# Optimization experiments

Measured on AMD Instinct MI355X. Metric: run time of the kernel, lower is better.

Reference implementation:

```python
import jax, jax.numpy as jnp
import numpy as np

B, H, W, CIN, F, KH, KW, E = 16, 112, 112, 128, 256, 3, 3, 3


@jax.custom_vjp
def ste_sign(x):
    # larq-style ste_sign: sign with sign(0) -> +1
    return jnp.where(x >= 0, 1.0, -1.0).astype(x.dtype)

def _ste_fwd(x):
    return ste_sign(x), x

def _ste_bwd(x, g):
    # straight-through estimator, clipped to |x| <= 1
    return (g * (jnp.abs(x) <= 1).astype(g.dtype),)

ste_sign.defvjp(_ste_fwd, _ste_bwd)


def conv2d(x, k):
    return jax.lax.conv_general_dilated(
        x, k, window_strides=(1, 1), padding='VALID',
        dimension_numbers=('NHWC', 'HWIO', 'NHWC'))


def setup_inputs() -> dict:
    key = jax.random.key(0)
    k1, k2 = jax.random.split(key)
    x = jax.random.normal(k1, (B, H, W, CIN), dtype=jnp.float32)
    kernels = jax.random.normal(k2, (E, KH, KW, CIN, F), dtype=jnp.float32) * 0.1
    # alpha initialized as mean |kernel| per output filter (as in build())
    alphas = jnp.mean(jnp.abs(kernels), axis=(1, 2, 3))  # [E, F]
    return {"x": x, "kernels": kernels, "alphas": alphas}


def reference(x, kernels, alphas):
    kh, kw, cin = kernels.shape[1], kernels.shape[2], kernels.shape[3]
    D = kh * kw * cin  # db_dimension
    xq = ste_sign(x)  # binarized input (shared across estimators)
    ones_k = jnp.ones((kh, kw, cin, 1), dtype=x.dtype)
    # beta: box-filter of |x| over window and channels, divided by D -> [B,H',W']
    beta = conv2d(jnp.abs(x), ones_k)[..., 0] / D
    out = jnp.zeros((1,), dtype=x.dtype)  # broadcast accumulator
    for e in range(kernels.shape[0]):
        Z = conv2d(xq, ste_sign(kernels[e]))  # [B,H',W',F], binary conv
        K = beta[..., None] * alphas[e]       # outer(beta, alpha)
        out = out + Z * K
    return out
```

## Files before the change

### kernel.cpp

```cpp
#include <hip/hip_runtime.h>
#include <hip/hip_bf16.h>
#include <stdint.h>

#define B_   16
#define H_   112
#define W_   112
#define CIN  128
#define F_   256
#define OH   110
#define OW   110
#define MTOT (B_*OH*OW)
#define KTOT 1152
#define PIX_IN (B_*H_*W_)
#define D_INV (1.0f/1152.0f)

typedef float floatx4 __attribute__((ext_vector_type(4)));
typedef int   intx4   __attribute__((ext_vector_type(4)));

typedef __attribute__((address_space(1))) uint32_t guint;
typedef __attribute__((address_space(3))) uint32_t luint;

__device__ __forceinline__ void gld_lds16(const void* g, void* l) {
    __builtin_amdgcn_global_load_lds((guint*)g, (luint*)l, 16, 0, 0);
}

#define WST_OFF   0
#define SF_OFF    294912
#define S_OFF     295936
#define BETA_OFF  1098752
#define XQ_OFF    1873152
#define NEED_FULL (XQ_OFF + (size_t)PIX_IN*CIN)

__global__ void prep_wq(const float* __restrict__ kern, const float* __restrict__ alph,
                        int8_t* __restrict__ wst, float* __restrict__ sf) {
    int idx = blockIdx.x * 256 + threadIdx.x;
    int r = idx >> 8, f = idx & 255;
    float a0 = alph[f], a1 = alph[256 + f], a2 = alph[512 + f];
    float w = 0.f;
    float kv0 = kern[idx], kv1 = kern[294912 + idx], kv2 = kern[589824 + idx];
    w += (__float_as_uint(kv0) & 0x80000000u) ? -a0 : a0;
    w += (__float_as_uint(kv1) & 0x80000000u) ? -a1 : a1;
    w += (__float_as_uint(kv2) & 0x80000000u) ? -a2 : a2;
    float s = (a0 + a1 + a2) * (1.0f / 127.0f);
    int q = (int)__builtin_rintf(w / s);
    wst[((((r >> 6) * 2 + (f >> 7)) * 4 + ((r >> 4) & 3)) * 128 + (f & 127)) * 16 + (r & 15)]
        = (int8_t)q;
    if (r == 0) sf[f] = s;
}

__device__ __forceinline__ uint32_t pack4sign(float4 v) {
    uint32_t b0 = ((__float_as_uint(v.x) >> 31) * 0xFEu) ^ 0x01u;
    uint32_t b1 = ((__float_as_uint(v.y) >> 31) * 0xFEu) ^ 0x01u;
    uint32_t b2 = ((__float_as_uint(v.z) >> 31) * 0xFEu) ^ 0x01u;
    uint32_t b3 = ((__float_as_uint(v.w) >> 31) * 0xFEu) ^ 0x01u;
    return b0 | (b1 << 8) | (b2 << 16) | (b3 << 24);
}

__global__ void prep_x(const float* __restrict__ x, uint32_t* __restrict__ xq,
                       float* __restrict__ S, int write_xq) {
    int idx = blockIdx.x * 256 + threadIdx.x;
    float4 v = ((const float4*)x)[idx];
    if (write_xq) xq[idx] = pack4sign(v);
    float s = fabsf(v.x) + fabsf(v.y) + fabsf(v.z) + fabsf(v.w);
#pragma unroll
    for (int o = 1; o < 32; o <<= 1) s += __shfl_xor(s, o, 64);
    if ((threadIdx.x & 31) == 0) S[idx >> 5] = s;
}

__global__ void prep_beta(const float* __restrict__ S, float* __restrict__ beta) {
    int m = blockIdx.x * 256 + threadIdx.x;
    if (m >= MTOT) return;
    int b = m / (OH * OW); int r = m - b * (OH * OW);
    int oi = r / OW, oj = r - oi * OW;
    const float* sp = S + (b * H_ + oi) * W_ + oj;
    float acc = 0.f;
#pragma unroll
    for (int dh = 0; dh < 3; ++dh)
#pragma unroll
        for (int dw = 0; dw < 3; ++dw) acc += sp[dh * W_ + dw];
    beta[m] = acc * D_INV;
}

template <bool PREBIN>
__global__ __launch_bounds__(256)
void conv_main(const void* __restrict__ xin, const int8_t* __restrict__ wst,
               const float* __restrict__ sf, const float* __restrict__ beta,
               float* __restrict__ out) {
    __shared__ char smem[16384];

    const int t = threadIdx.x;
    const int l = t & 63, wv = t >> 6;
    const int quad = l >> 4, lane16 = l & 15;
    const int wm = wv >> 1, wn = wv & 1;
    const int f0 = blockIdx.x * 128;
    const int m0 = blockIdx.y * 128;

    const char* a_base[2];
    const char* b_base[2];
#pragma unroll
    for (int q = 0; q < 2; ++q) {
        int idx = q * 256 + t;
        int chunk = idx >> 7, rn = idx & 127;
        int m = m0 + rn; if (m >= MTOT) m = MTOT - 1;
        int b = m / (OH * OW); int rr = m - b * (OH * OW);
        int oi = rr / OW, oj = rr - oi * OW;
        long pix = ((long)(b * H_ + oi) * W_ + oj) * CIN;
        a_base[q] = (const char*)xin + (PREBIN ? (pix + chunk * 16)
                                               : (pix + chunk * 16) * 4);
        b_base[q] = (const char*)wst + blockIdx.x * 8192 + idx * 16;
    }

    intx4 acc[4][4];
#pragma unroll
    for (int a = 0; a < 4; ++a)
#pragma unroll
        for (int bb = 0; bb < 4; ++bb) acc[a][bb] = (intx4){0, 0, 0, 0};

    for (int ks = 0; ks < 18; ++ks) {
        int kh = ks / 6, rem = ks - kh * 6;
        int kw = rem >> 1, c0 = (rem & 1) << 6;
        int aoff = (kh * W_ + kw) * CIN + c0;
#pragma unroll
        for (int q = 0; q < 2; ++q) {
            int idx = q * 256 + t;
            if (PREBIN) {
                gld_lds16(a_base[q] + aoff, smem + idx * 16);
            } else {
                const float4* src = (const float4*)(a_base[q] + (long)aoff * 4);
                float4 v0 = src[0], v1 = src[1], v2 = src[2], v3 = src[3];
                uint4 pv = make_uint4(pack4sign(v0), pack4sign(v1),
                                      pack4sign(v2), pack4sign(v3));
                *(uint4*)(smem + idx * 16) = pv;
            }
            gld_lds16(b_base[q] + (long)ks * 16384, smem + 8192 + idx * 16);
        }
        __syncthreads();

        intx4 af[4], bf[4];
#pragma unroll
        for (int tm = 0; tm < 4; ++tm) {
            int row = wm * 64 + tm * 16 + lane16;
            af[tm] = *(const intx4*)(smem + quad * 2048 + row * 16);
        }
#pragma unroll
        for (int tn = 0; tn < 4; ++tn) {
            int col = wn * 64 + tn * 16 + lane16;
            bf[tn] = *(const intx4*)(smem + 8192 + quad * 2048 + col * 16);
        }
#pragma unroll
        for (int tm = 0; tm < 4; ++tm)
#pragma unroll
            for (int tn = 0; tn < 4; ++tn)
                acc[tm][tn] = __builtin_amdgcn_mfma_i32_16x16x64_i8(
                    af[tm], bf[tn], acc[tm][tn], 0, 0, 0);
        __syncthreads();
    }

    float sv[4];
#pragma unroll
    for (int tn = 0; tn < 4; ++tn) sv[tn] = sf[f0 + wn * 64 + tn * 16 + lane16];

#pragma unroll
    for (int tm = 0; tm < 4; ++tm) {
#pragma unroll
        for (int i = 0; i < 4; ++i) {
            int m = m0 + wm * 64 + tm * 16 + quad * 4 + i;
            if (m < MTOT) {
                float bv = beta[m];
                float* op = out + (long)m * F_ + f0 + wn * 64 + lane16;
#pragma unroll
                for (int tn = 0; tn < 4; ++tn)
                    op[tn * 16] = (float)acc[tm][tn][i] * (bv * sv[tn]);
            }
        }
    }
}

extern "C" void kernel_launch(void* const* d_in, const int* in_sizes, int n_in,
                              void* d_out, int out_size, void* d_ws, size_t ws_size,
                              hipStream_t stream) {
    const float* x    = (const float*)d_in[0];
    const float* kern = (const float*)d_in[1];
    const float* alph = (const float*)d_in[2];
    float* out = (float*)d_out;
    char* ws = (char*)d_ws;

    int8_t* wst  = (int8_t*)(ws + WST_OFF);
    float*  sf   = (float*)(ws + SF_OFF);
    float*  S    = (float*)(ws + S_OFF);
    float*  beta = (float*)(ws + BETA_OFF);
    char*   xq   = ws + XQ_OFF;
    bool prebin = ws_size >= NEED_FULL;

    hipLaunchKernelGGL(prep_wq, dim3(KTOT * F_ / 256), dim3(256), 0, stream,
                       kern, alph, wst, sf);
    hipLaunchKernelGGL(prep_x, dim3(PIX_IN * CIN / 4 / 256), dim3(256), 0, stream,
                       x, (uint32_t*)xq, S, (int)prebin);
    hipLaunchKernelGGL(prep_beta, dim3((MTOT + 255) / 256), dim3(256), 0, stream, S, beta);

    dim3 grid(2, (MTOT + 127) / 128);
    if (prebin)
        hipLaunchKernelGGL(conv_main<true>, grid, dim3(256), 0, stream,
                           (const void*)xq, wst, sf, beta, out);
    else
        hipLaunchKernelGGL(conv_main<false>, grid, dim3(256), 0, stream,
                           (const void*)x, wst, sf, beta, out);
}
```

Measured before the change: 352.4 us.

## Double-buffer LDS tiles in binary conv GEMM and remap workgroups per XCD

```diff
diff --git a/kernel.cpp b/kernel.cpp
--- a/kernel.cpp
+++ b/kernel.cpp
@@ -86,28 +86,35 @@
 void conv_main(const void* __restrict__ xin, const int8_t* __restrict__ wst,
                const float* __restrict__ sf, const float* __restrict__ beta,
                float* __restrict__ out) {
-    __shared__ char smem[16384];
+    __shared__ char smem[32768];
 
     const int t = threadIdx.x;
     const int l = t & 63, wv = t >> 6;
     const int quad = l >> 4, lane16 = l & 15;
     const int wm = wv >> 1, wn = wv & 1;
-    const int f0 = blockIdx.x * 128;
-    const int m0 = blockIdx.y * 128;
+
+    const int nwg  = gridDim.x * gridDim.y;
+    const int wgid = blockIdx.y * gridDim.x + blockIdx.x;
+    const int qn = nwg >> 3, rn = nwg & 7;
+    const int xcd = wgid & 7, ii = wgid >> 3;
+    const int nid = (xcd < rn ? xcd * (qn + 1) : rn * (qn + 1) + (xcd - rn) * qn) + ii;
+    const int f0 = (nid & 1) * 128;
+    const int m0 = (nid >> 1) * 128;
+    const int fblk = nid & 1;
 
     const char* a_base[2];
     const char* b_base[2];
 #pragma unroll
     for (int q = 0; q < 2; ++q) {
         int idx = q * 256 + t;
-        int chunk = idx >> 7, rn = idx & 127;
-        int m = m0 + rn; if (m >= MTOT) m = MTOT - 1;
+        int chunk = idx >> 7, rnn = idx & 127;
+        int m = m0 + rnn; if (m >= MTOT) m = MTOT - 1;
         int b = m / (OH * OW); int rr = m - b * (OH * OW);
         int oi = rr / OW, oj = rr - oi * OW;
         long pix = ((long)(b * H_ + oi) * W_ + oj) * CIN;
         a_base[q] = (const char*)xin + (PREBIN ? (pix + chunk * 16)
                                                : (pix + chunk * 16) * 4);
-        b_base[q] = (const char*)wst + blockIdx.x * 8192 + idx * 16;
+        b_base[q] = (const char*)wst + fblk * 8192 + idx * 16;
     }
 
     intx4 acc[4][4];
@@ -116,44 +123,65 @@
 #pragma unroll
         for (int bb = 0; bb < 4; ++bb) acc[a][bb] = (intx4){0, 0, 0, 0};
 
-    for (int ks = 0; ks < 18; ++ks) {
+    auto STAGE = [&](int ks, int buf) {
         int kh = ks / 6, rem = ks - kh * 6;
         int kw = rem >> 1, c0 = (rem & 1) << 6;
         int aoff = (kh * W_ + kw) * CIN + c0;
+        char* dst = smem + buf * 16384;
 #pragma unroll
         for (int q = 0; q < 2; ++q) {
             int idx = q * 256 + t;
             if (PREBIN) {
-                gld_lds16(a_base[q] + aoff, smem + idx * 16);
+                gld_lds16(a_base[q] + aoff, dst + idx * 16);
             } else {
                 const float4* src = (const float4*)(a_base[q] + (long)aoff * 4);
                 float4 v0 = src[0], v1 = src[1], v2 = src[2], v3 = src[3];
                 uint4 pv = make_uint4(pack4sign(v0), pack4sign(v1),
                                       pack4sign(v2), pack4sign(v3));
-                *(uint4*)(smem + idx * 16) = pv;
+                *(uint4*)(dst + idx * 16) = pv;
             }
-            gld_lds16(b_base[q] + (long)ks * 16384, smem + 8192 + idx * 16);
-        }
-        __syncthreads();
-
+            gld_lds16(b_base[q] + (long)ks * 16384, dst + 8192 + idx * 16);
+        }
+    };
+
+    STAGE(0, 0);
+
+    for (int ks = 0; ks < 18; ++ks) {
+        const int cur = ks & 1;
+        if (ks < 17) {
+            STAGE(ks + 1, cur ^ 1);
+            if (PREBIN)
+                asm volatile("s_waitcnt vmcnt(4)\ns_barrier" ::: "memory");
+            else
+                __syncthreads();
+        } else {
+            if (PREBIN)
+                asm volatile("s_waitcnt vmcnt(0)\ns_barrier" ::: "memory");
+            else
+                __syncthreads();
+        }
+
+        const char* sbase = smem + cur * 16384;
         intx4 af[4], bf[4];
 #pragma unroll
         for (int tm = 0; tm < 4; ++tm) {
             int row = wm * 64 + tm * 16 + lane16;
-            af[tm] = *(const intx4*)(smem + quad * 2048 + row * 16);
+            af[tm] = *(const intx4*)(sbase + quad * 2048 + row * 16);
         }
 #pragma unroll
         for (int tn = 0; tn < 4; ++tn) {
             int col = wn * 64 + tn * 16 + lane16;
-            bf[tn] = *(const intx4*)(smem + 8192 + quad * 2048 + col * 16);
-        }
+            bf[tn] = *(const intx4*)(sbase + 8192 + quad * 2048 + col * 16);
+        }
+        __builtin_amdgcn_s_setprio(1);
 #pragma unroll
         for (int tm = 0; tm < 4; ++tm)
 #pragma unroll
             for (int tn = 0; tn < 4; ++tn)
                 acc[tm][tn] = __builtin_amdgcn_mfma_i32_16x16x64_i8(
                     af[tm], bf[tn], acc[tm][tn], 0, 0, 0);
-        __syncthreads();
+        __builtin_amdgcn_s_setprio(0);
+        asm volatile("s_barrier" ::: "memory");
     }
 
     float sv[4];
```

After: 335.2 us. 1.05x faster.
